# Performance work log

Measured on AMD Instinct MI355X. Metric: run time of the kernel, lower is better.

The kernel has to match this reference:

```python
import jax, jax.numpy as jnp
import numpy as np

N_NODES = 50000
N_EDGES = 800000
IN_CH = 64
HID = 128
EPS = 1e-12  # F.normalize default eps


def setup_inputs() -> dict:
    key = jax.random.key(0)
    ks = jax.random.split(key, 12)
    x = jax.random.normal(ks[0], (N_NODES, IN_CH), dtype=jnp.float32)
    edge_index = jax.random.randint(ks[1], (2, N_EDGES), 0, N_NODES, dtype=jnp.int64)
    def lin(k, out_c, in_c):
        bound = 1.0 / np.sqrt(in_c)
        return jax.random.uniform(k, (out_c, in_c), jnp.float32, -bound, bound)
    # layer 0: in->hid ; layers 1,2: hid->hid
    Wl0 = lin(ks[2], HID, IN_CH); bl0 = jnp.zeros((HID,), jnp.float32); Wr0 = lin(ks[3], HID, IN_CH)
    Wl1 = lin(ks[4], HID, HID);  bl1 = jnp.zeros((HID,), jnp.float32); Wr1 = lin(ks[5], HID, HID)
    Wl2 = lin(ks[6], HID, HID);  bl2 = jnp.zeros((HID,), jnp.float32); Wr2 = lin(ks[7], HID, HID)
    return {"x": x, "edge_index": edge_index,
            "Wl0": Wl0, "bl0": bl0, "Wr0": Wr0,
            "Wl1": Wl1, "bl1": bl1, "Wr1": Wr1,
            "Wl2": Wl2, "bl2": bl2, "Wr2": Wr2}


def _sage_conv(h, src, dst, Wl, bl, Wr, n_nodes):
    # mean aggregation of source-node features at target nodes
    msg = h[src]                                                   # [E, d]
    agg = jax.ops.segment_sum(msg, dst, num_segments=n_nodes)      # [N, d]
    cnt = jax.ops.segment_sum(jnp.ones((src.shape[0],), h.dtype), dst,
                              num_segments=n_nodes)                # [N]
    mean = agg / jnp.maximum(cnt, 1.0)[:, None]
    out = mean @ Wl.T + bl + h @ Wr.T                              # lin_l(agg)+lin_r(x)
    # L2 normalize (F.normalize, p=2)
    norm = jnp.maximum(jnp.linalg.norm(out, axis=-1, keepdims=True), EPS)
    return out / norm


def reference(x, edge_index, Wl0, bl0, Wr0, Wl1, bl1, Wr1, Wl2, bl2, Wr2):
    src, dst = edge_index[0], edge_index[1]
    n = x.shape[0]
    h = _sage_conv(x, src, dst, Wl0, bl0, Wr0, n)
    h = jax.nn.relu(h)  # dropout is identity in eval mode
    h = _sage_conv(h, src, dst, Wl1, bl1, Wr1, n)
    h = jax.nn.relu(h)
    h = _sage_conv(h, src, dst, Wl2, bl2, Wr2, n)
    return h
```

## Files before the change

### kernel.cpp

```cpp
#include <hip/hip_runtime.h>

#define NN 50000
#define NNP 50016
#define NE 800000
#define DIN 64
#define HD 128
#define NBUK 196
#define SB 196
#define BCAP 12288

typedef __attribute__((ext_vector_type(8))) short short8;
typedef __attribute__((ext_vector_type(4))) float f32x4;
typedef __attribute__((ext_vector_type(4))) unsigned short us4;
typedef __attribute__((ext_vector_type(8))) unsigned short us8;

__device__ __forceinline__ unsigned short f2bf(float f) {
    unsigned int u = __float_as_uint(f);
    u = (u + 0x7FFFu + ((u >> 16) & 1u)) >> 16;
    return (unsigned short)u;
}
__device__ __forceinline__ float bf2f(unsigned short u) {
    return __uint_as_float(((unsigned int)u) << 16);
}

#define LDS_SCAN256(a, t)                                 \
    for (int off_ = 1; off_ < 256; off_ <<= 1) {          \
        int add_ = ((t) >= off_) ? (a)[(t) - off_] : 0;   \
        __syncthreads();                                  \
        (a)[t] += add_;                                   \
        __syncthreads();                                  \
    }


__global__ void zero_meta(int* __restrict__ meta) {
    meta[threadIdx.x] = 0;
}

__global__ __launch_bounds__(256) void bucket_count(const int* __restrict__ dst,
                                                    int* __restrict__ bcnt) {
    __shared__ int lc[256];
    int t = threadIdx.x;
    lc[t] = 0;
    __syncthreads();
    int base = blockIdx.x * 4096 + t * 16;
#pragma unroll
    for (int j = 0; j < 4; ++j) {
        int e = base + j * 4;
        if (e < NE) {
            int4 d = *(const int4*)(dst + e);
            atomicAdd(&lc[d.x >> 8], 1);
            atomicAdd(&lc[d.y >> 8], 1);
            atomicAdd(&lc[d.z >> 8], 1);
            atomicAdd(&lc[d.w >> 8], 1);
        }
    }
    __syncthreads();
    if (t < NBUK && lc[t] > 0) atomicAdd(&bcnt[t], lc[t]);
}

__global__ __launch_bounds__(256) void bucket_scan(const int* __restrict__ bcnt,
                                                   int* __restrict__ bbase,
                                                   int* __restrict__ rowptr) {
    __shared__ int sh[256];
    int t = threadIdx.x;
    int v = (t < NBUK) ? bcnt[t] : 0;
    sh[t] = v;
    __syncthreads();
    LDS_SCAN256(sh, t);
    if (t < NBUK) bbase[t] = sh[t] - v;
    if (t == NBUK - 1) bbase[NBUK] = sh[t];
    if (t == 0) rowptr[NN] = NE;
}

__global__ __launch_bounds__(256) void bucket_scatter(
    const int* __restrict__ src, const int* __restrict__ dst,
    const int* __restrict__ bbase, int* __restrict__ bfill,
    int2* __restrict__ pairs) {
    __shared__ int cnt[256];
    __shared__ int incl[256];
    __shared__ int lfill[256];
    __shared__ int rung[256];
    __shared__ int2 buf[4096];
    int t = threadIdx.x;
    cnt[t] = 0;
    lfill[t] = 0;
    __syncthreads();
    int base = blockIdx.x * 4096 + t * 16;
#pragma unroll
    for (int j = 0; j < 4; ++j) {
        int e = base + j * 4;
        if (e < NE) {
            int4 d = *(const int4*)(dst + e);
            atomicAdd(&cnt[d.x >> 8], 1);
            atomicAdd(&cnt[d.y >> 8], 1);
            atomicAdd(&cnt[d.z >> 8], 1);
            atomicAdd(&cnt[d.w >> 8], 1);
        }
    }
    __syncthreads();
    incl[t] = cnt[t];
    __syncthreads();
    LDS_SCAN256(incl, t);
    int c = cnt[t];
    if (t < NBUK && c > 0) rung[t] = bbase[t] + atomicAdd(&bfill[t], c);
    __syncthreads();
#pragma unroll
    for (int j = 0; j < 4; ++j) {
        int e = base + j * 4;
        if (e < NE) {
            int4 s4 = *(const int4*)(src + e);
            int4 d4 = *(const int4*)(dst + e);
            int ss[4] = {s4.x, s4.y, s4.z, s4.w};
            int dd[4] = {d4.x, d4.y, d4.z, d4.w};
#pragma unroll
            for (int q = 0; q < 4; ++q) {
                int k = dd[q] >> 8;
                int p = (incl[k] - cnt[k]) + atomicAdd(&lfill[k], 1);
                buf[p] = {ss[q], dd[q]};
            }
        }
    }
    __syncthreads();
    int n = min(4096, NE - blockIdx.x * 4096);
    for (int i = t; i < n; i += 256) {
        int2 pr = buf[i];
        int k = pr.y >> 8;
        pairs[rung[k] + (i - (incl[k] - cnt[k]))] = pr;
    }
}

__global__ __launch_bounds__(256) void build_csr(
    const int2* __restrict__ pairs, const int* __restrict__ bbase,
    int* __restrict__ rowptr, float* __restrict__ invcnt,
    int* __restrict__ csr_src) {
    __shared__ int cnt[256];
    __shared__ int incl[256];
    __shared__ int lfill[256];
    __shared__ int sbuf[BCAP];
    int b = blockIdx.x, t = threadIdx.x;
    int pbeg = bbase[b], pend = bbase[b + 1];
    int sz = pend - pbeg;
    cnt[t] = 0;
    lfill[t] = 0;
    __syncthreads();
    for (int i = t; i < sz; i += 256)
        atomicAdd(&cnt[pairs[pbeg + i].y & 255], 1);
    __syncthreads();
    incl[t] = cnt[t];
    __syncthreads();
    LDS_SCAN256(incl, t);
    int node = b * 256 + t;
    int c = cnt[t];
    if (node < NN) {
        rowptr[node] = pbeg + incl[t] - c;
        invcnt[node] = 1.0f / (float)(c > 0 ? c : 1);
    }
    if (sz <= BCAP) {
        for (int i = t; i < sz; i += 256) {
            int2 pr = pairs[pbeg + i];
            int ld = pr.y & 255;
            sbuf[(incl[ld] - cnt[ld]) + atomicAdd(&lfill[ld], 1)] = pr.x;
        }
        __syncthreads();
        for (int i = t; i < sz; i += 256) csr_src[pbeg + i] = sbuf[i];
    } else {
        for (int i = t; i < sz; i += 256) {
            int2 pr = pairs[pbeg + i];
            int ld = pr.y & 255;
            csr_src[pbeg + (incl[ld] - cnt[ld]) + atomicAdd(&lfill[ld], 1)] = pr.x;
        }
    }
}


__device__ __forceinline__ void pack_one(const float* Wl, const float* Wr, int D,
                                         unsigned short* Wpk, int i) {
    int j = i & 7;
    int lane = (i >> 3) & 63;
    int ct = (i >> 9) & 7;
    int ks = i >> 12;
    int k = ks * 32 + ((lane >> 4) << 3) + j;
    int c = ct * 16 + (lane & 15);
    float v = (k < D) ? Wl[c * D + k] : Wr[c * D + (k - D)];
    Wpk[i] = f2bf(v);
}

__global__ void pack_weights(const float* __restrict__ Wl0, const float* __restrict__ Wr0,
                             const float* __restrict__ Wl1, const float* __restrict__ Wr1,
                             const float* __restrict__ Wl2, const float* __restrict__ Wr2,
                             unsigned short* __restrict__ Wpk0,
                             unsigned short* __restrict__ Wpk1,
                             unsigned short* __restrict__ Wpk2) {
    const int S0 = 2 * DIN * HD;
    const int S12 = 2 * HD * HD;
    int i = blockIdx.x * blockDim.x + threadIdx.x;
    if (i < S0) { pack_one(Wl0, Wr0, DIN, Wpk0, i); return; }
    int j = i - S0;
    if (j < S12) { pack_one(Wl1, Wr1, HD, Wpk1, j); return; }
    int m = j - S12;
    if (m < S12) pack_one(Wl2, Wr2, HD, Wpk2, m);
}

__global__ void conv_x(const float* __restrict__ x, unsigned short* __restrict__ A0) {
    int i = blockIdx.x * blockDim.x + threadIdx.x;
    if (i >= NN * 16) return;
    int row = i >> 4, c4 = i & 15;
    float4 v = ((const float4*)(x + (size_t)row * DIN))[c4];
    us4 o = {f2bf(v.x), f2bf(v.y), f2bf(v.z), f2bf(v.w)};
    *(us4*)(A0 + (size_t)row * 128 + 64 + c4 * 4) = o;
}


__global__ __launch_bounds__(256) void gather_mean_x(
    const int* __restrict__ rowptr, const int* __restrict__ csr_src,
    const float* __restrict__ invcnt, unsigned short* __restrict__ A0) {
    int tid = threadIdx.x;
    int n = blockIdx.x * 4 + (tid >> 6);
    int lane = tid & 63;
    int c8 = lane & 7;
    int g = lane >> 3;
    int beg = rowptr[n], end = rowptr[n + 1];
    float acc[8] = {};
    const unsigned short* hb = A0 + 64 + (size_t)c8 * 8;
    int e = beg + g;
    for (; e + 8 < end; e += 16) {
        int s0 = csr_src[e], s1 = csr_src[e + 8];
        us8 v0 = *(const us8*)(hb + (size_t)s0 * 128);
        us8 v1 = *(const us8*)(hb + (size_t)s1 * 128);
#pragma unroll
        for (int j = 0; j < 8; ++j) acc[j] += bf2f(v0[j]) + bf2f(v1[j]);
    }
    if (e < end) {
        us8 v0 = *(const us8*)(hb + (size_t)csr_src[e] * 128);
#pragma unroll
        for (int j = 0; j < 8; ++j) acc[j] += bf2f(v0[j]);
    }
#pragma unroll
    for (int j = 0; j < 8; ++j) {
        acc[j] += __shfl_xor(acc[j], 8, 64);
        acc[j] += __shfl_xor(acc[j], 16, 64);
        acc[j] += __shfl_xor(acc[j], 32, 64);
    }
    if (g == 0) {
        float ic = invcnt[n];
        us8 o;
#pragma unroll
        for (int j = 0; j < 8; ++j) o[j] = f2bf(acc[j] * ic);
        *(us8*)(A0 + (size_t)n * 128 + c8 * 8) = o;
    }
}


__global__ __launch_bounds__(256) void gather_mean_h(
    const unsigned short* __restrict__ A12, const int* __restrict__ rowptr,
    const int* __restrict__ csr_src, const float* __restrict__ invcnt,
    unsigned short* __restrict__ Am) {
    int tid = threadIdx.x;
    int n = blockIdx.x * 4 + (tid >> 6);
    int lane = tid & 63;
    int c8 = lane & 15;
    int g = lane >> 4;
    int beg = rowptr[n], end = rowptr[n + 1];
    float acc[8] = {};
    const unsigned short* hb = A12 + 128 + (size_t)c8 * 8;
    int e = beg + g;
    for (; e + 4 < end; e += 8) {
        int s0 = csr_src[e], s1 = csr_src[e + 4];
        us8 v0 = *(const us8*)(hb + (size_t)s0 * 256);
        us8 v1 = *(const us8*)(hb + (size_t)s1 * 256);
#pragma unroll
        for (int j = 0; j < 8; ++j) acc[j] += bf2f(v0[j]) + bf2f(v1[j]);
    }
    if (e < end) {
        us8 v0 = *(const us8*)(hb + (size_t)csr_src[e] * 256);
#pragma unroll
        for (int j = 0; j < 8; ++j) acc[j] += bf2f(v0[j]);
    }
#pragma unroll
    for (int j = 0; j < 8; ++j) {
        acc[j] += __shfl_xor(acc[j], 16, 64);
        acc[j] += __shfl_xor(acc[j], 32, 64);
    }
    if (g == 0) {
        float ic = invcnt[n];
        us8 o;
#pragma unroll
        for (int j = 0; j < 8; ++j) o[j] = f2bf(acc[j] * ic);
        *(us8*)(Am + (size_t)n * 256 + c8 * 8) = o;
    }
}


template <int K, bool RELU, bool F32OUT, bool BF16H>
__global__ __launch_bounds__(256) void linear_mfma(
    const unsigned short* __restrict__ A, const unsigned short* __restrict__ Wpk,
    const float* __restrict__ bias, float* __restrict__ outF,
    unsigned short* __restrict__ Hn ) {
    constexpr int NK = K / 32;
    __shared__ float rsum[2][32];
    int tid = threadIdx.x;
    int lane = tid & 63, w = tid >> 6;
    int rg = w >> 1, cg = w & 1;
    int r0 = blockIdx.x * 32 + rg * 16;
    int row_l = lane & 15, kb = lane >> 4;

    const unsigned short* Arow = A + (size_t)(r0 + row_l) * K + kb * 8;
    const unsigned short* Wp = Wpk + ((size_t)(cg * 4) * 64 + lane) * 8;

    f32x4 acc[4] = {{0.f, 0.f, 0.f, 0.f}, {0.f, 0.f, 0.f, 0.f},
                    {0.f, 0.f, 0.f, 0.f}, {0.f, 0.f, 0.f, 0.f}};
#pragma unroll
    for (int ks = 0; ks < NK; ++ks) {
        short8 a = *(const short8*)(Arow + ks * 32);
#pragma unroll
        for (int t = 0; t < 4; ++t) {
            short8 b = *(const short8*)(Wp + ((size_t)ks * 8 + t) * 64 * 8);
            acc[t] = __builtin_amdgcn_mfma_f32_16x16x32_bf16(a, b, acc[t], 0, 0, 0);
        }
    }

    float sq[4] = {0.f, 0.f, 0.f, 0.f};
#pragma unroll
    for (int t = 0; t < 4; ++t) {
        float bv = bias[cg * 64 + t * 16 + row_l];
#pragma unroll
        for (int r = 0; r < 4; ++r) {
            acc[t][r] += bv;
            sq[r] = fmaf(acc[t][r], acc[t][r], sq[r]);
        }
    }
#pragma unroll
    for (int off = 1; off < 16; off <<= 1)
#pragma unroll
        for (int r = 0; r < 4; ++r) sq[r] += __shfl_xor(sq[r], off, 64);

    if (row_l == 0) {
#pragma unroll
        for (int r = 0; r < 4; ++r) rsum[cg][rg * 16 + kb * 4 + r] = sq[r];
    }
    __syncthreads();

    int rbase = rg * 16 + kb * 4;
#pragma unroll
    for (int r = 0; r < 4; ++r) {
        int row = r0 + kb * 4 + r;
        if (row >= NN) continue;
        float n2 = rsum[0][rbase + r] + rsum[1][rbase + r];
        float inv = 1.0f / fmaxf(sqrtf(n2), 1e-12f);
#pragma unroll
        for (int t = 0; t < 4; ++t) {
            float v = acc[t][r] * inv;
            if (RELU) v = fmaxf(v, 0.f);
            int c = cg * 64 + t * 16 + row_l;
            if (F32OUT) outF[(size_t)row * HD + c] = v;
            if (BF16H) Hn[(size_t)row * 256 + c] = f2bf(v);
        }
    }
}


static inline size_t align256(size_t x) { return (x + 255) & ~(size_t)255; }

extern "C" void kernel_launch(void* const* d_in, const int* in_sizes, int n_in,
                              void* d_out, int out_size, void* d_ws, size_t ws_size,
                              hipStream_t stream) {
    const float* x   = (const float*)d_in[0];
    const int*   ei  = (const int*)d_in[1];
    const float* Wl0 = (const float*)d_in[2];
    const float* bl0 = (const float*)d_in[3];
    const float* Wr0 = (const float*)d_in[4];
    const float* Wl1 = (const float*)d_in[5];
    const float* bl1 = (const float*)d_in[6];
    const float* Wr1 = (const float*)d_in[7];
    const float* Wl2 = (const float*)d_in[8];
    const float* bl2 = (const float*)d_in[9];
    const float* Wr2 = (const float*)d_in[10];

    const int* src = ei;
    const int* dst = ei + NE;

    char* p = (char*)d_ws;
    size_t off = 0;
    int* meta = (int*)(p + off);            off = align256(off + 512 * 4);
    int* bbase = (int*)(p + off);           off = align256(off + 256 * 4);
    int* rowptr = (int*)(p + off);          off = align256(off + (size_t)(NN + 1) * 4);
    int* csr_src = (int*)(p + off);         off = align256(off + (size_t)NE * 4);
    float* invcnt = (float*)(p + off);      off = align256(off + (size_t)NN * 4);
    int2* pairs = (int2*)(p + off);         off = align256(off + (size_t)NE * 8);
    unsigned short* A0 = (unsigned short*)(p + off);   off = align256(off + (size_t)NNP * 128 * 2);
    unsigned short* A12 = (unsigned short*)(p + off);  off = align256(off + (size_t)NNP * 256 * 2);
    unsigned short* Wpk0 = (unsigned short*)(p + off); off = align256(off + (size_t)2 * DIN * HD * 2);
    unsigned short* Wpk1 = (unsigned short*)(p + off); off = align256(off + (size_t)2 * HD * HD * 2);
    unsigned short* Wpk2 = (unsigned short*)(p + off); off = align256(off + (size_t)2 * HD * HD * 2);
    (void)ws_size; (void)n_in; (void)in_sizes; (void)out_size;

    int* bcnt = meta;
    int* bfill = meta + 256;
    float* out = (float*)d_out;

    zero_meta<<<1, 512, 0, stream>>>(meta);
    bucket_count<<<SB, 256, 0, stream>>>(dst, bcnt);
    bucket_scan<<<1, 256, 0, stream>>>(bcnt, bbase, rowptr);
    bucket_scatter<<<SB, 256, 0, stream>>>(src, dst, bbase, bfill, pairs);
    build_csr<<<NBUK, 256, 0, stream>>>(pairs, bbase, rowptr, invcnt, csr_src);

    const int WTOT = 2 * DIN * HD + 2 * 2 * HD * HD;
    pack_weights<<<(WTOT + 255) / 256, 256, 0, stream>>>(Wl0, Wr0, Wl1, Wr1, Wl2, Wr2,
                                                         Wpk0, Wpk1, Wpk2);
    conv_x<<<(NN * 16 + 255) / 256, 256, 0, stream>>>(x, A0);

    const int LG = NNP / 32;
    const int GG = NN / 4;

    gather_mean_x<<<GG, 256, 0, stream>>>(rowptr, csr_src, invcnt, A0);
    linear_mfma<2 * DIN, true, false, true><<<LG, 256, 0, stream>>>(
        A0, Wpk0, bl0, nullptr, A12 + 128);

    gather_mean_h<<<GG, 256, 0, stream>>>(A12, rowptr, csr_src, invcnt, A12);
    linear_mfma<2 * HD, true, false, true><<<LG, 256, 0, stream>>>(
        A12, Wpk1, bl1, nullptr, A12 + 128);

    gather_mean_h<<<GG, 256, 0, stream>>>(A12, rowptr, csr_src, invcnt, A12);
    linear_mfma<2 * HD, false, true, false><<<LG, 256, 0, stream>>>(
        A12, Wpk2, bl2, out, nullptr);
}
```

Before: 176.0 us.

## Pack edge pairs into 32-bit words, merge prep kernels, retune gather kernels

Edge pairs go from int2 to one 32-bit word holding the low 8 bits of dst and a 24-bit src. This halves the pairs traffic in scatter and CSR build. Weight packing, x conversion and meta zeroing are merged into one prep kernel, which saves two launches. The gather kernels now use 32 threads per node for the x layer and are unrolled four ways over edges for more memory-level parallelism. The packing assumes node ids fit in 24 bits.

```diff
diff --git a/kernel.cpp b/kernel.cpp
--- a/kernel.cpp
+++ b/kernel.cpp
@@ -32,10 +32,6 @@
     }
 
 
-__global__ void zero_meta(int* __restrict__ meta) {
-    meta[threadIdx.x] = 0;
-}
-
 __global__ __launch_bounds__(256) void bucket_count(const int* __restrict__ dst,
                                                     int* __restrict__ bcnt) {
     __shared__ int lc[256];
@@ -75,12 +71,13 @@
 __global__ __launch_bounds__(256) void bucket_scatter(
     const int* __restrict__ src, const int* __restrict__ dst,
     const int* __restrict__ bbase, int* __restrict__ bfill,
-    int2* __restrict__ pairs) {
+    int* __restrict__ pairs) {
     __shared__ int cnt[256];
     __shared__ int incl[256];
     __shared__ int lfill[256];
     __shared__ int rung[256];
-    __shared__ int2 buf[4096];
+    __shared__ int buf[4096];
+    __shared__ unsigned char bk[4096];
     int t = threadIdx.x;
     cnt[t] = 0;
     lfill[t] = 0;
@@ -116,21 +113,21 @@
             for (int q = 0; q < 4; ++q) {
                 int k = dd[q] >> 8;
                 int p = (incl[k] - cnt[k]) + atomicAdd(&lfill[k], 1);
-                buf[p] = {ss[q], dd[q]};
+                buf[p] = ((dd[q] & 255) << 24) | ss[q];
+                bk[p] = (unsigned char)k;
             }
         }
     }
     __syncthreads();
     int n = min(4096, NE - blockIdx.x * 4096);
     for (int i = t; i < n; i += 256) {
-        int2 pr = buf[i];
-        int k = pr.y >> 8;
-        pairs[rung[k] + (i - (incl[k] - cnt[k]))] = pr;
+        int k = bk[i];
+        pairs[rung[k] + (i - (incl[k] - cnt[k]))] = buf[i];
     }
 }
 
 __global__ __launch_bounds__(256) void build_csr(
-    const int2* __restrict__ pairs, const int* __restrict__ bbase,
+    const int* __restrict__ pairs, const int* __restrict__ bbase,
     int* __restrict__ rowptr, float* __restrict__ invcnt,
     int* __restrict__ csr_src) {
     __shared__ int cnt[256];
@@ -144,7 +141,7 @@
     lfill[t] = 0;
     __syncthreads();
     for (int i = t; i < sz; i += 256)
-        atomicAdd(&cnt[pairs[pbeg + i].y & 255], 1);
+        atomicAdd(&cnt[(unsigned)pairs[pbeg + i] >> 24], 1);
     __syncthreads();
     incl[t] = cnt[t];
     __syncthreads();
@@ -157,17 +154,17 @@
     }
     if (sz <= BCAP) {
         for (int i = t; i < sz; i += 256) {
-            int2 pr = pairs[pbeg + i];
-            int ld = pr.y & 255;
-            sbuf[(incl[ld] - cnt[ld]) + atomicAdd(&lfill[ld], 1)] = pr.x;
+            int pr = pairs[pbeg + i];
+            int ld = (unsigned)pr >> 24;
+            sbuf[(incl[ld] - cnt[ld]) + atomicAdd(&lfill[ld], 1)] = pr & 0xFFFFFF;
         }
         __syncthreads();
         for (int i = t; i < sz; i += 256) csr_src[pbeg + i] = sbuf[i];
     } else {
         for (int i = t; i < sz; i += 256) {
-            int2 pr = pairs[pbeg + i];
-            int ld = pr.y & 255;
-            csr_src[pbeg + (incl[ld] - cnt[ld]) + atomicAdd(&lfill[ld], 1)] = pr.x;
+            int pr = pairs[pbeg + i];
+            int ld = (unsigned)pr >> 24;
+            csr_src[pbeg + (incl[ld] - cnt[ld]) + atomicAdd(&lfill[ld], 1)] = pr & 0xFFFFFF;
         }
     }
 }
@@ -185,29 +182,40 @@
     Wpk[i] = f2bf(v);
 }
 
-__global__ void pack_weights(const float* __restrict__ Wl0, const float* __restrict__ Wr0,
-                             const float* __restrict__ Wl1, const float* __restrict__ Wr1,
-                             const float* __restrict__ Wl2, const float* __restrict__ Wr2,
-                             unsigned short* __restrict__ Wpk0,
-                             unsigned short* __restrict__ Wpk1,
-                             unsigned short* __restrict__ Wpk2) {
+#define PACK_BLOCKS 320
+#define CONV_BLOCKS 3125
+
+__global__ __launch_bounds__(256) void prep(
+    const float* __restrict__ Wl0, const float* __restrict__ Wr0,
+    const float* __restrict__ Wl1, const float* __restrict__ Wr1,
+    const float* __restrict__ Wl2, const float* __restrict__ Wr2,
+    unsigned short* __restrict__ Wpk0, unsigned short* __restrict__ Wpk1,
+    unsigned short* __restrict__ Wpk2,
+    const float* __restrict__ x, unsigned short* __restrict__ A0,
+    int* __restrict__ meta) {
     const int S0 = 2 * DIN * HD;
     const int S12 = 2 * HD * HD;
-    int i = blockIdx.x * blockDim.x + threadIdx.x;
-    if (i < S0) { pack_one(Wl0, Wr0, DIN, Wpk0, i); return; }
-    int j = i - S0;
-    if (j < S12) { pack_one(Wl1, Wr1, HD, Wpk1, j); return; }
-    int m = j - S12;
-    if (m < S12) pack_one(Wl2, Wr2, HD, Wpk2, m);
-}
-
-__global__ void conv_x(const float* __restrict__ x, unsigned short* __restrict__ A0) {
-    int i = blockIdx.x * blockDim.x + threadIdx.x;
-    if (i >= NN * 16) return;
-    int row = i >> 4, c4 = i & 15;
-    float4 v = ((const float4*)(x + (size_t)row * DIN))[c4];
-    us4 o = {f2bf(v.x), f2bf(v.y), f2bf(v.z), f2bf(v.w)};
-    *(us4*)(A0 + (size_t)row * 128 + 64 + c4 * 4) = o;
+    int b = blockIdx.x;
+    int t = threadIdx.x;
+    if (b < PACK_BLOCKS) {
+        int i = b * 256 + t;
+        if (i < S0) { pack_one(Wl0, Wr0, DIN, Wpk0, i); return; }
+        int j = i - S0;
+        if (j < S12) { pack_one(Wl1, Wr1, HD, Wpk1, j); return; }
+        int m = j - S12;
+        if (m < S12) pack_one(Wl2, Wr2, HD, Wpk2, m);
+        return;
+    }
+    if (b < PACK_BLOCKS + CONV_BLOCKS) {
+        int i = (b - PACK_BLOCKS) * 256 + t;
+        int row = i >> 4, c4 = i & 15;
+        float4 v = ((const float4*)(x + (size_t)row * DIN))[c4];
+        us4 o = {f2bf(v.x), f2bf(v.y), f2bf(v.z), f2bf(v.w)};
+        *(us4*)(A0 + (size_t)row * 128 + 64 + c4 * 4) = o;
+        return;
+    }
+    meta[t] = 0;
+    meta[t + 256] = 0;
 }
 
 
@@ -215,22 +223,24 @@
     const int* __restrict__ rowptr, const int* __restrict__ csr_src,
     const float* __restrict__ invcnt, unsigned short* __restrict__ A0) {
     int tid = threadIdx.x;
-    int n = blockIdx.x * 4 + (tid >> 6);
-    int lane = tid & 63;
-    int c8 = lane & 7;
-    int g = lane >> 3;
+    int n = blockIdx.x * 8 + (tid >> 5);
+    int c8 = tid & 7;
+    int eg = (tid >> 3) & 3;
     int beg = rowptr[n], end = rowptr[n + 1];
     float acc[8] = {};
     const unsigned short* hb = A0 + 64 + (size_t)c8 * 8;
-    int e = beg + g;
-    for (; e + 8 < end; e += 16) {
-        int s0 = csr_src[e], s1 = csr_src[e + 8];
-        us8 v0 = *(const us8*)(hb + (size_t)s0 * 128);
-        us8 v1 = *(const us8*)(hb + (size_t)s1 * 128);
-#pragma unroll
-        for (int j = 0; j < 8; ++j) acc[j] += bf2f(v0[j]) + bf2f(v1[j]);
-    }
-    if (e < end) {
+    int e = beg + eg;
+    for (; e + 12 < end; e += 16) {
+        int i0 = csr_src[e], i1 = csr_src[e + 4], i2 = csr_src[e + 8], i3 = csr_src[e + 12];
+        us8 v0 = *(const us8*)(hb + (size_t)i0 * 128);
+        us8 v1 = *(const us8*)(hb + (size_t)i1 * 128);
+        us8 v2 = *(const us8*)(hb + (size_t)i2 * 128);
+        us8 v3 = *(const us8*)(hb + (size_t)i3 * 128);
+#pragma unroll
+        for (int j = 0; j < 8; ++j)
+            acc[j] += (bf2f(v0[j]) + bf2f(v1[j])) + (bf2f(v2[j]) + bf2f(v3[j]));
+    }
+    for (; e < end; e += 4) {
         us8 v0 = *(const us8*)(hb + (size_t)csr_src[e] * 128);
 #pragma unroll
         for (int j = 0; j < 8; ++j) acc[j] += bf2f(v0[j]);
@@ -239,9 +249,8 @@
     for (int j = 0; j < 8; ++j) {
         acc[j] += __shfl_xor(acc[j], 8, 64);
         acc[j] += __shfl_xor(acc[j], 16, 64);
-        acc[j] += __shfl_xor(acc[j], 32, 64);
-    }
-    if (g == 0) {
+    }
+    if (eg == 0) {
         float ic = invcnt[n];
         us8 o;
 #pragma unroll
@@ -259,19 +268,22 @@
     int n = blockIdx.x * 4 + (tid >> 6);
     int lane = tid & 63;
     int c8 = lane & 15;
-    int g = lane >> 4;
+    int eg = lane >> 4;
     int beg = rowptr[n], end = rowptr[n + 1];
     float acc[8] = {};
     const unsigned short* hb = A12 + 128 + (size_t)c8 * 8;
-    int e = beg + g;
-    for (; e + 4 < end; e += 8) {
-        int s0 = csr_src[e], s1 = csr_src[e + 4];
-        us8 v0 = *(const us8*)(hb + (size_t)s0 * 256);
-        us8 v1 = *(const us8*)(hb + (size_t)s1 * 256);
-#pragma unroll
-        for (int j = 0; j < 8; ++j) acc[j] += bf2f(v0[j]) + bf2f(v1[j]);
-    }
-    if (e < end) {
+    int e = beg + eg;
+    for (; e + 12 < end; e += 16) {
+        int i0 = csr_src[e], i1 = csr_src[e + 4], i2 = csr_src[e + 8], i3 = csr_src[e + 12];
+        us8 v0 = *(const us8*)(hb + (size_t)i0 * 256);
+        us8 v1 = *(const us8*)(hb + (size_t)i1 * 256);
+        us8 v2 = *(const us8*)(hb + (size_t)i2 * 256);
+        us8 v3 = *(const us8*)(hb + (size_t)i3 * 256);
+#pragma unroll
+        for (int j = 0; j < 8; ++j)
+            acc[j] += (bf2f(v0[j]) + bf2f(v1[j])) + (bf2f(v2[j]) + bf2f(v3[j]));
+    }
+    for (; e < end; e += 4) {
         us8 v0 = *(const us8*)(hb + (size_t)csr_src[e] * 256);
 #pragma unroll
         for (int j = 0; j < 8; ++j) acc[j] += bf2f(v0[j]);
@@ -281,7 +293,7 @@
         acc[j] += __shfl_xor(acc[j], 16, 64);
         acc[j] += __shfl_xor(acc[j], 32, 64);
     }
-    if (g == 0) {
+    if (eg == 0) {
         float ic = invcnt[n];
         us8 o;
 #pragma unroll
@@ -386,7 +398,7 @@
     int* rowptr = (int*)(p + off);          off = align256(off + (size_t)(NN + 1) * 4);
     int* csr_src = (int*)(p + off);         off = align256(off + (size_t)NE * 4);
     float* invcnt = (float*)(p + off);      off = align256(off + (size_t)NN * 4);
-    int2* pairs = (int2*)(p + off);         off = align256(off + (size_t)NE * 8);
+    int* pairs = (int*)(p + off);           off = align256(off + (size_t)NE * 4);
     unsigned short* A0 = (unsigned short*)(p + off);   off = align256(off + (size_t)NNP * 128 * 2);
     unsigned short* A12 = (unsigned short*)(p + off);  off = align256(off + (size_t)NNP * 256 * 2);
     unsigned short* Wpk0 = (unsigned short*)(p + off); off = align256(off + (size_t)2 * DIN * HD * 2);
@@ -398,29 +410,27 @@
     int* bfill = meta + 256;
     float* out = (float*)d_out;
 
-    zero_meta<<<1, 512, 0, stream>>>(meta);
+    prep<<<PACK_BLOCKS + CONV_BLOCKS + 1, 256, 0, stream>>>(
+        Wl0, Wr0, Wl1, Wr1, Wl2, Wr2, Wpk0, Wpk1, Wpk2, x, A0, meta);
+
     bucket_count<<<SB, 256, 0, stream>>>(dst, bcnt);
     bucket_scan<<<1, 256, 0, stream>>>(bcnt, bbase, rowptr);
     bucket_scatter<<<SB, 256, 0, stream>>>(src, dst, bbase, bfill, pairs);
     build_csr<<<NBUK, 256, 0, stream>>>(pairs, bbase, rowptr, invcnt, csr_src);
 
-    const int WTOT = 2 * DIN * HD + 2 * 2 * HD * HD;
-    pack_weights<<<(WTOT + 255) / 256, 256, 0, stream>>>(Wl0, Wr0, Wl1, Wr1, Wl2, Wr2,
-                                                         Wpk0, Wpk1, Wpk2);
-    conv_x<<<(NN * 16 + 255) / 256, 256, 0, stream>>>(x, A0);
-
     const int LG = NNP / 32;
-    const int GG = NN / 4;
-
-    gather_mean_x<<<GG, 256, 0, stream>>>(rowptr, csr_src, invcnt, A0);
+    const int GX = NN / 8;
+    const int GH = NN / 4;
+
+    gather_mean_x<<<GX, 256, 0, stream>>>(rowptr, csr_src, invcnt, A0);
     linear_mfma<2 * DIN, true, false, true><<<LG, 256, 0, stream>>>(
         A0, Wpk0, bl0, nullptr, A12 + 128);
 
-    gather_mean_h<<<GG, 256, 0, stream>>>(A12, rowptr, csr_src, invcnt, A12);
+    gather_mean_h<<<GH, 256, 0, stream>>>(A12, rowptr, csr_src, invcnt, A12);
     linear_mfma<2 * HD, true, false, true><<<LG, 256, 0, stream>>>(
         A12, Wpk1, bl1, nullptr, A12 + 128);
 
-    gather_mean_h<<<GG, 256, 0, stream>>>(A12, rowptr, csr_src, invcnt, A12);
+    gather_mean_h<<<GH, 256, 0, stream>>>(A12, rowptr, csr_src, invcnt, A12);
     linear_mfma<2 * HD, false, true, false><<<LG, 256, 0, stream>>>(
         A12, Wpk2, bl2, out, nullptr);
 }
```

After: 166.8 us. 5.2% less time.
